# Kernel optimization log

Measured on AMD Instinct MI355X. Metric: run time of the kernel, lower is better.

Reference implementation:

```python
import jax, jax.numpy as jnp
import numpy as np

HT_H, HT_W = 512, 512          # Hough accumulator grid
SPHERE_SIZE = 32768            # Gaussian-sphere bins
NUM_VOTES = 1_500_000          # rows in vote_mapping
BATCH, CHANNEL = 2, 64         # channel % 4 == 0 required by the module


def setup_inputs() -> dict:
    key = jax.random.key(0)
    k1, k2, k3, k4 = jax.random.split(key, 4)
    x = jax.random.normal(k1, (BATCH, CHANNEL, HT_H, HT_W), dtype=jnp.float32)
    ht_idx = jax.random.randint(k2, (NUM_VOTES,), 0, HT_H * HT_W, dtype=jnp.int32)
    sphere_idx = jax.random.randint(k3, (NUM_VOTES,), 0, SPHERE_SIZE, dtype=jnp.int32)
    weight = jax.random.uniform(k4, (NUM_VOTES,), dtype=jnp.float32)
    return {"x": x, "ht_idx": ht_idx, "sphere_idx": sphere_idx, "weight": weight}


def reference(x, ht_idx, sphere_idx, weight):
    b, c, h, w = x.shape
    # SPHERE_CUDA.forward: split channels into 4 groups, flatten HT grid
    xf = x.reshape(b * 4, c // 4, h * w)              # [B4, C4, HW]
    # HT2SPHERE: gather each vote's HT cell, scale by vote weight,
    # scatter-add into its sphere bin.
    votes = xf[:, :, ht_idx] * weight                  # [B4, C4, V]
    out = jax.ops.segment_sum(
        jnp.moveaxis(votes, -1, 0), sphere_idx, num_segments=SPHERE_SIZE
    )                                                  # [S, B4, C4]
    out = jnp.moveaxis(out, 0, -1)                     # [B4, C4, S]
    return out.reshape(b, c, SPHERE_SIZE)              # [B, C, S]
```

## Files before the change

### kernel.cpp

```cpp
#include <hip/hip_runtime.h>
#include <stdint.h>


#define S_BINS   32768
#define NBUCKET  1024
#define BINS     32
#define CAP      2048
#define CHUNK    4096
#define HT_BITS  18

__device__ __forceinline__ unsigned bf16_rne(float f) {
    unsigned u = __float_as_uint(f);
    return (u + 0x7FFFu + ((u >> 16) & 1u)) >> 16;
}

__global__ void transpose_x_bf16_kernel(const float* __restrict__ x,
                                        uint32_t* __restrict__ xTb, int HW) {
    __shared__ float tile[64][129];
    const int ht0 = blockIdx.x * 64;
    const int tid = threadIdx.x;
    for (int e = tid; e < 128 * 64; e += 256) {
        const int ch = e >> 6, hl = e & 63;
        tile[hl][ch] = x[(size_t)ch * HW + ht0 + hl];
    }
    __syncthreads();
    for (int e = tid; e < 64 * 64; e += 256) {
        const int hl = e >> 6, cp = e & 63;
        const unsigned lo = bf16_rne(tile[hl][cp]);
        const unsigned hi = bf16_rne(tile[hl][cp + 64]);
        xTb[(size_t)(ht0 + hl) * 64 + cp] = lo | (hi << 16);
    }
}

__global__ void init_kernel(int* __restrict__ cursor, int* __restrict__ spillCnt) {
    const int t = threadIdx.x;
    cursor[t] = t * CAP;
    if (t == 0) *spillCnt = 0;
}

__global__ __launch_bounds__(512) void reorder_kernel(
    const int* __restrict__ ht, const int* __restrict__ sp,
    const float* __restrict__ w, int* __restrict__ cursor,
    uint2* __restrict__ records, uint2* __restrict__ spillRec,
    int* __restrict__ spillBkt, int* __restrict__ spillCnt, int V) {
    __shared__ uint2 rec[CHUNK];
    __shared__ uint16_t bid[CHUNK];
    __shared__ uint16_t sval[CHUNK];
    __shared__ int hist[NBUCKET], start[NBUCKET], cur[NBUCKET], gbase[NBUCKET];
    __shared__ int psum[512];
    const int blk = blockIdx.x, t = threadIdx.x;
    const int base = blk * CHUNK, end = min(V, base + CHUNK), n = end - base;
    hist[2 * t] = 0; hist[2 * t + 1] = 0;
    __syncthreads();
    for (int v = base + t; v < end; v += 512) {
        const int s = sp[v];
        sval[v - base] = (uint16_t)s;
        atomicAdd(&hist[s >> 5], 1);
    }
    __syncthreads();
    const int l0 = hist[2 * t], l1 = hist[2 * t + 1];
    psum[t] = l0 + l1;
    __syncthreads();
    for (int off = 1; off < 512; off <<= 1) {
        const int add = (t >= off) ? psum[t - off] : 0;
        __syncthreads();
        psum[t] += add;
        __syncthreads();
    }
    int run = (t == 0) ? 0 : psum[t - 1];
    start[2 * t]     = run; cur[2 * t]     = run; run += l0;
    start[2 * t + 1] = run; cur[2 * t + 1] = run;
    if (l0) gbase[2 * t]     = atomicAdd(&cursor[2 * t],     l0);
    if (l1) gbase[2 * t + 1] = atomicAdd(&cursor[2 * t + 1], l1);
    __syncthreads();
    for (int v = base + t; v < end; v += 512) {
        const int s = (int)sval[v - base];
        const int b = s >> 5, sl = s & 31;
        const int pos = atomicAdd(&cur[b], 1);
        rec[pos] = make_uint2((unsigned)ht[v] | ((unsigned)sl << HT_BITS),
                              __float_as_uint(w[v]));
        bid[pos] = (uint16_t)b;
    }
    __syncthreads();
    for (int i = t; i < n; i += 512) {
        const int b = bid[i];
        const int slot = gbase[b] + (i - start[b]);
        if (slot < (b + 1) * CAP) {
            records[slot] = rec[i];
        } else {
            const int pos = atomicAdd(spillCnt, 1);
            spillRec[pos] = rec[i];
            spillBkt[pos] = b;
        }
    }
}

__global__ __launch_bounds__(512) void accum_kernel(
    const uint32_t* __restrict__ xTb, const uint2* __restrict__ records,
    const int* __restrict__ cursor, const uint2* __restrict__ spillRec,
    const int* __restrict__ spillBkt, const int* __restrict__ spillCnt,
    float* __restrict__ out) {
    __shared__ uint2 sorted[CAP];
    __shared__ __align__(16) char rawbuf[BINS * 129 * 4];
    __shared__ int hist[BINS], off[BINS + 1], cur[BINS];
    uint2* raw = (uint2*)rawbuf;
    const uint4* xTb4 = (const uint4*)xTb;
    const int bkt = blockIdx.x, t = threadIdx.x;
    const int lane = t & 63, wv = t >> 6;
    const int q = lane >> 4, ql = lane & 15;
    const int n = min(cursor[bkt] - bkt * CAP, CAP);
    const int rbase = bkt * CAP;
    float a[4][8];
#pragma unroll
    for (int i = 0; i < 4; ++i)
#pragma unroll
        for (int j = 0; j < 8; ++j) a[i][j] = 0.f;

    if (t < BINS) hist[t] = 0;
    __syncthreads();
    for (int i = t; i < n; i += 512) {
        const uint2 r = records[rbase + i];
        raw[i] = r;
        atomicAdd(&hist[(r.x >> HT_BITS) & 31], 1);
    }
    __syncthreads();
    if (t == 0) {
        int run = 0;
        for (int j = 0; j < BINS; ++j) { off[j] = run; cur[j] = run; run += hist[j]; }
        off[BINS] = run;
    }
    __syncthreads();
    for (int i = t; i < n; i += 512) {
        const uint2 r = raw[i];
        const int pos = atomicAdd(&cur[(r.x >> HT_BITS) & 31], 1);
        sorted[pos] = r;
    }
    __syncthreads();
#pragma unroll
    for (int bb = 0; bb < 4; ++bb) {
        const int f = wv * 4 + bb;
        const int s0 = off[f], s1 = off[f + 1];
#pragma unroll 1
        for (int k = s0; k < s1; k += 16) {
#pragma unroll
            for (int u = 0; u < 4; ++u) {
                const int kk = k + 4 * u + q;
                if (kk < s1) {
                    const uint2 r = sorted[kk];
                    const uint4 g = xTb4[(size_t)(r.x & 0x3FFFF) * 16 + ql];
                    const float wt = __uint_as_float(r.y);
                    a[bb][0] += __uint_as_float(g.x << 16)          * wt;
                    a[bb][1] += __uint_as_float(g.x & 0xFFFF0000u)  * wt;
                    a[bb][2] += __uint_as_float(g.y << 16)          * wt;
                    a[bb][3] += __uint_as_float(g.y & 0xFFFF0000u)  * wt;
                    a[bb][4] += __uint_as_float(g.z << 16)          * wt;
                    a[bb][5] += __uint_as_float(g.z & 0xFFFF0000u)  * wt;
                    a[bb][6] += __uint_as_float(g.w << 16)          * wt;
                    a[bb][7] += __uint_as_float(g.w & 0xFFFF0000u)  * wt;
                }
            }
        }
    }
#pragma unroll
    for (int bb = 0; bb < 4; ++bb)
#pragma unroll
        for (int j = 0; j < 8; ++j) {
            a[bb][j] += __shfl_xor(a[bb][j], 16);
            a[bb][j] += __shfl_xor(a[bb][j], 32);
        }
    __syncthreads();
    float* epi = (float*)rawbuf;
    if (lane < 16) {
#pragma unroll
        for (int bb = 0; bb < 4; ++bb) {
            const int f = wv * 4 + bb;
            epi[f * 129 + 4 * ql]      = a[bb][0];
            epi[f * 129 + 4 * ql + 64] = a[bb][1];
            epi[f * 129 + 4 * ql + 1]  = a[bb][2];
            epi[f * 129 + 4 * ql + 65] = a[bb][3];
            epi[f * 129 + 4 * ql + 2]  = a[bb][4];
            epi[f * 129 + 4 * ql + 66] = a[bb][5];
            epi[f * 129 + 4 * ql + 3]  = a[bb][6];
            epi[f * 129 + 4 * ql + 67] = a[bb][7];
        }
    }
    __syncthreads();
    const int cnt = *spillCnt;
    if (cnt > 0) {
        const uint2* xTb2 = (const uint2*)xTb;
        const int hl = lane & 31;
        for (int i = t >> 5; i < cnt; i += 16) {
            if (spillBkt[i] == bkt) {
                const uint2 r = spillRec[i];
                const int f = (r.x >> HT_BITS) & 31;
                const uint2 g = xTb2[(size_t)(r.x & 0x3FFFF) * 32 + hl];
                const float wt = __uint_as_float(r.y);
                atomicAdd(&epi[f * 129 + 2 * hl],
                          __uint_as_float(g.x << 16) * wt);
                atomicAdd(&epi[f * 129 + 2 * hl + 64],
                          __uint_as_float(g.x & 0xFFFF0000u) * wt);
                atomicAdd(&epi[f * 129 + 2 * hl + 1],
                          __uint_as_float(g.y << 16) * wt);
                atomicAdd(&epi[f * 129 + 2 * hl + 65],
                          __uint_as_float(g.y & 0xFFFF0000u) * wt);
            }
        }
        __syncthreads();
    }
    for (int i = t; i < 128 * BINS; i += 512) {
        const int ch = i >> 5, bin = i & 31;
        out[(size_t)ch * S_BINS + bkt * BINS + bin] = epi[bin * 129 + ch];
    }
}

__global__ void direct_kernel(const float* __restrict__ x,
                              const int* __restrict__ ht_idx,
                              const int* __restrict__ sp_idx,
                              const float* __restrict__ weight,
                              float* __restrict__ out, int V, int HW, int S,
                              int CH) {
    const int v = blockIdx.x * 2 + (threadIdx.x >> 7);
    if (v >= V) return;
    const int ch = threadIdx.x & 127;
    if (ch >= CH) return;
    atomicAdd(&out[(size_t)ch * S + sp_idx[v]],
              x[(size_t)ch * HW + ht_idx[v]] * weight[v]);
}

extern "C" void kernel_launch(void* const* d_in, const int* in_sizes, int n_in,
                              void* d_out, int out_size, void* d_ws, size_t ws_size,
                              hipStream_t stream) {
    const float* x  = (const float*)d_in[0];
    const int*   ht = (const int*)d_in[1];
    const int*   sp = (const int*)d_in[2];
    const float* w  = (const float*)d_in[3];
    float* out = (float*)d_out;

    const int HW = 512 * 512;
    const int CH = in_sizes[0] / HW;
    const int S  = out_size / CH;
    const int V  = in_sizes[1];
    const int nblk = (V + CHUNK - 1) / CHUNK;

    const size_t xTb_bytes = (size_t)CH * HW * sizeof(uint16_t);
    const size_t rec_bytes = (size_t)NBUCKET * CAP * sizeof(uint2);
    const size_t spr_bytes = (size_t)V * sizeof(uint2);
    const size_t spb_bytes = (size_t)V * sizeof(int);
    const size_t cur_bytes = (size_t)NBUCKET * sizeof(int);
    const size_t cnt_bytes = 64;
    const size_t need = xTb_bytes + rec_bytes + spr_bytes + spb_bytes +
                        cur_bytes + cnt_bytes;

    if (CH == 128 && S == S_BINS && HW == (1 << HT_BITS) && ws_size >= need) {
        char* p = (char*)d_ws;
        uint32_t* xTb  = (uint32_t*)p;  p += xTb_bytes;
        uint2* records = (uint2*)p;     p += rec_bytes;
        uint2* spillRec= (uint2*)p;     p += spr_bytes;
        int* spillBkt  = (int*)p;       p += spb_bytes;
        int* cursor    = (int*)p;       p += cur_bytes;
        int* spillCnt  = (int*)p;

        init_kernel<<<1, NBUCKET, 0, stream>>>(cursor, spillCnt);
        transpose_x_bf16_kernel<<<HW / 64, 256, 0, stream>>>(x, xTb, HW);
        reorder_kernel<<<nblk, 512, 0, stream>>>(ht, sp, w, cursor, records,
                                                 spillRec, spillBkt, spillCnt, V);
        accum_kernel<<<NBUCKET, 512, 0, stream>>>(xTb, records, cursor,
                                                  spillRec, spillBkt, spillCnt,
                                                  out);
    } else {
        hipMemsetAsync(out, 0, (size_t)out_size * sizeof(float), stream);
        direct_kernel<<<(V + 1) / 2, 256, 0, stream>>>(x, ht, sp, w, out, V, HW,
                                                       S, CH);
    }
}
```

Measured before the change: 314.8 us.

## Merge transpose and vote-reorder kernels into one launch with shared smem

Combines the bf16 transpose of x and the bucket-reorder of votes into a single kernel, with block ranges split by blockIdx so both independent jobs run concurrently and one launch is saved. The reorder chunk size is halved so the shared-memory union fits in about 38 KB, and the cached sp copy in shared memory is dropped in favour of re-reading sp from global. The transpose blocks now use 512 threads. Smaller chunks double the number of reorder blocks, which means more global cursor atomics and smaller contiguous runs per bucket in the records write.

```diff
diff --git a/kernel.cpp b/kernel.cpp
--- a/kernel.cpp
+++ b/kernel.cpp
@@ -6,30 +6,12 @@
 #define NBUCKET  1024
 #define BINS     32
 #define CAP      2048
-#define CHUNK    4096
+#define CHUNK    2048
 #define HT_BITS  18
 
 __device__ __forceinline__ unsigned bf16_rne(float f) {
     unsigned u = __float_as_uint(f);
     return (u + 0x7FFFu + ((u >> 16) & 1u)) >> 16;
-}
-
-__global__ void transpose_x_bf16_kernel(const float* __restrict__ x,
-                                        uint32_t* __restrict__ xTb, int HW) {
-    __shared__ float tile[64][129];
-    const int ht0 = blockIdx.x * 64;
-    const int tid = threadIdx.x;
-    for (int e = tid; e < 128 * 64; e += 256) {
-        const int ch = e >> 6, hl = e & 63;
-        tile[hl][ch] = x[(size_t)ch * HW + ht0 + hl];
-    }
-    __syncthreads();
-    for (int e = tid; e < 64 * 64; e += 256) {
-        const int hl = e >> 6, cp = e & 63;
-        const unsigned lo = bf16_rne(tile[hl][cp]);
-        const unsigned hi = bf16_rne(tile[hl][cp + 64]);
-        xTb[(size_t)(ht0 + hl) * 64 + cp] = lo | (hi << 16);
-    }
 }
 
 __global__ void init_kernel(int* __restrict__ cursor, int* __restrict__ spillCnt) {
@@ -38,59 +20,77 @@
     if (t == 0) *spillCnt = 0;
 }
 
-__global__ __launch_bounds__(512) void reorder_kernel(
+__global__ __launch_bounds__(512) void fused_tr_kernel(
+    const float* __restrict__ x, uint32_t* __restrict__ xTb, int HW,
     const int* __restrict__ ht, const int* __restrict__ sp,
     const float* __restrict__ w, int* __restrict__ cursor,
     uint2* __restrict__ records, uint2* __restrict__ spillRec,
-    int* __restrict__ spillBkt, int* __restrict__ spillCnt, int V) {
-    __shared__ uint2 rec[CHUNK];
-    __shared__ uint16_t bid[CHUNK];
-    __shared__ uint16_t sval[CHUNK];
-    __shared__ int hist[NBUCKET], start[NBUCKET], cur[NBUCKET], gbase[NBUCKET];
-    __shared__ int psum[512];
-    const int blk = blockIdx.x, t = threadIdx.x;
-    const int base = blk * CHUNK, end = min(V, base + CHUNK), n = end - base;
-    hist[2 * t] = 0; hist[2 * t + 1] = 0;
-    __syncthreads();
-    for (int v = base + t; v < end; v += 512) {
-        const int s = sp[v];
-        sval[v - base] = (uint16_t)s;
-        atomicAdd(&hist[s >> 5], 1);
-    }
-    __syncthreads();
-    const int l0 = hist[2 * t], l1 = hist[2 * t + 1];
-    psum[t] = l0 + l1;
-    __syncthreads();
-    for (int off = 1; off < 512; off <<= 1) {
-        const int add = (t >= off) ? psum[t - off] : 0;
-        __syncthreads();
-        psum[t] += add;
-        __syncthreads();
-    }
-    int run = (t == 0) ? 0 : psum[t - 1];
-    start[2 * t]     = run; cur[2 * t]     = run; run += l0;
-    start[2 * t + 1] = run; cur[2 * t + 1] = run;
-    if (l0) gbase[2 * t]     = atomicAdd(&cursor[2 * t],     l0);
-    if (l1) gbase[2 * t + 1] = atomicAdd(&cursor[2 * t + 1], l1);
-    __syncthreads();
-    for (int v = base + t; v < end; v += 512) {
-        const int s = (int)sval[v - base];
-        const int b = s >> 5, sl = s & 31;
-        const int pos = atomicAdd(&cur[b], 1);
-        rec[pos] = make_uint2((unsigned)ht[v] | ((unsigned)sl << HT_BITS),
-                              __float_as_uint(w[v]));
-        bid[pos] = (uint16_t)b;
-    }
-    __syncthreads();
-    for (int i = t; i < n; i += 512) {
-        const int b = bid[i];
-        const int slot = gbase[b] + (i - start[b]);
-        if (slot < (b + 1) * CAP) {
-            records[slot] = rec[i];
-        } else {
-            const int pos = atomicAdd(spillCnt, 1);
-            spillRec[pos] = rec[i];
-            spillBkt[pos] = b;
+    int* __restrict__ spillBkt, int* __restrict__ spillCnt,
+    int V, int nrb) {
+    __shared__ __align__(16) char smem[38912];
+    const int t = threadIdx.x;
+    if ((int)blockIdx.x < nrb) {
+        uint2*    rec   = (uint2*)smem;
+        uint16_t* bid   = (uint16_t*)(smem + 16384);
+        int*      hist  = (int*)(smem + 20480);
+        int*      start = (int*)(smem + 24576);
+        int*      cur   = (int*)(smem + 28672);
+        int*      gbase = (int*)(smem + 32768);
+        int*      psum  = (int*)(smem + 36864);
+        const int blk = blockIdx.x;
+        const int base = blk * CHUNK, end = min(V, base + CHUNK), n = end - base;
+        hist[2 * t] = 0; hist[2 * t + 1] = 0;
+        __syncthreads();
+        for (int v = base + t; v < end; v += 512) atomicAdd(&hist[sp[v] >> 5], 1);
+        __syncthreads();
+        const int l0 = hist[2 * t], l1 = hist[2 * t + 1];
+        psum[t] = l0 + l1;
+        __syncthreads();
+        for (int off = 1; off < 512; off <<= 1) {
+            const int add = (t >= off) ? psum[t - off] : 0;
+            __syncthreads();
+            psum[t] += add;
+            __syncthreads();
+        }
+        int run = (t == 0) ? 0 : psum[t - 1];
+        start[2 * t]     = run; cur[2 * t]     = run; run += l0;
+        start[2 * t + 1] = run; cur[2 * t + 1] = run;
+        if (l0) gbase[2 * t]     = atomicAdd(&cursor[2 * t],     l0);
+        if (l1) gbase[2 * t + 1] = atomicAdd(&cursor[2 * t + 1], l1);
+        __syncthreads();
+        for (int v = base + t; v < end; v += 512) {
+            const int s = sp[v];
+            const int b = s >> 5, sl = s & 31;
+            const int pos = atomicAdd(&cur[b], 1);
+            rec[pos] = make_uint2((unsigned)ht[v] | ((unsigned)sl << HT_BITS),
+                                  __float_as_uint(w[v]));
+            bid[pos] = (uint16_t)b;
+        }
+        __syncthreads();
+        for (int i = t; i < n; i += 512) {
+            const int b = bid[i];
+            const int slot = gbase[b] + (i - start[b]);
+            if (slot < (b + 1) * CAP) {
+                records[slot] = rec[i];
+            } else {
+                const int pos = atomicAdd(spillCnt, 1);
+                spillRec[pos] = rec[i];
+                spillBkt[pos] = b;
+            }
+        }
+    } else {
+        float* tile = (float*)smem;
+        const int ht0 = ((int)blockIdx.x - nrb) * 64;
+        for (int e = t; e < 128 * 64; e += 512) {
+            const int ch = e >> 6, hl = e & 63;
+            tile[hl * 129 + ch] = x[(size_t)ch * HW + ht0 + hl];
+        }
+        __syncthreads();
+        for (int e = t; e < 64 * 64; e += 512) {
+            const int hl = e >> 6, cp = e & 63;
+            const unsigned lo = bf16_rne(tile[hl * 129 + cp]);
+            const unsigned hi = bf16_rne(tile[hl * 129 + cp + 64]);
+            xTb[(size_t)(ht0 + hl) * 64 + cp] = lo | (hi << 16);
         }
     }
 }
@@ -240,7 +240,8 @@
     const int CH = in_sizes[0] / HW;
     const int S  = out_size / CH;
     const int V  = in_sizes[1];
-    const int nblk = (V + CHUNK - 1) / CHUNK;
+    const int nrb = (V + CHUNK - 1) / CHUNK;
+    const int ntb = HW / 64;
 
     const size_t xTb_bytes = (size_t)CH * HW * sizeof(uint16_t);
     const size_t rec_bytes = (size_t)NBUCKET * CAP * sizeof(uint2);
@@ -261,9 +262,9 @@
         int* spillCnt  = (int*)p;
 
         init_kernel<<<1, NBUCKET, 0, stream>>>(cursor, spillCnt);
-        transpose_x_bf16_kernel<<<HW / 64, 256, 0, stream>>>(x, xTb, HW);
-        reorder_kernel<<<nblk, 512, 0, stream>>>(ht, sp, w, cursor, records,
-                                                 spillRec, spillBkt, spillCnt, V);
+        fused_tr_kernel<<<nrb + ntb, 512, 0, stream>>>(
+            x, xTb, HW, ht, sp, w, cursor, records, spillRec, spillBkt,
+            spillCnt, V, nrb);
         accum_kernel<<<NBUCKET, 512, 0, stream>>>(xTb, records, cursor,
                                                   spillRec, spillBkt, spillCnt,
                                                   out);
```

After: 319.5 us. No clear change (+1.5%).
